# Performance work log

Measured on AMD Instinct MI355X. Metric: run time of the kernel, lower is better.

## Reference

```python
import jax, jax.numpy as jnp
import numpy as np

H = 8
LN_EPS = 1e-5

def setup_inputs() -> dict:
    key = jax.random.key(0)
    k1, k2, k3, k4 = jax.random.split(key, 4)
    bh, q_len, dk = 64, 1024, 64
    return {
        "query": jax.random.normal(k1, (bh, q_len, dk), dtype=jnp.float32),
        "key": jax.random.normal(k2, (bh, q_len, dk), dtype=jnp.float32),
        "value": jax.random.normal(k3, (bh, q_len, dk), dtype=jnp.float32),
        "head_att": jax.random.normal(k4, (H, H), dtype=jnp.float32),
        "ln_w": jnp.ones((H,), dtype=jnp.float32),
        "ln_b": jnp.zeros((H,), dtype=jnp.float32),
    }

def reference(query, key, value, head_att, ln_w, ln_b):
    bh, q_len, dk = query.shape
    k_len = key.shape[1]
    # scores: (bh, q, k)
    scores = jnp.einsum("bqd,bkd->bqk", query, key) / jnp.sqrt(jnp.asarray(dk, query.dtype))
    attn = jax.nn.softmax(scores, axis=-1)
    # view as (B, H, q, k) then move heads last: (B, q, k, H)
    a = attn.reshape(-1, H, q_len, k_len).transpose(0, 2, 3, 1)
    # DeepViT re-attention: cross-head mixing matmul
    a = a @ head_att  # (B, q, k, H)
    # LayerNorm over head dim
    mu = a.mean(axis=-1, keepdims=True)
    var = ((a - mu) ** 2).mean(axis=-1, keepdims=True)
    a = (a - mu) * jax.lax.rsqrt(var + LN_EPS) * ln_w + ln_b
    # back to (B, H, q, k)
    a = a.transpose(0, 3, 1, 2)
    att_map = a.mean(axis=1)  # (B, q, k)
    attention = a.reshape(bh, q_len, k_len)
    out = jnp.einsum("bqk,bkd->bqd", attention, value)
    return (out, att_map)
```

## Files before the change

### kernel.cpp

```cpp
#include <hip/hip_runtime.h>
#include <hip/hip_bf16.h>

typedef _Float16 f16;
typedef f16 f16x8 __attribute__((ext_vector_type(8)));
typedef f16 f16x4 __attribute__((ext_vector_type(4)));
typedef float f32x4 __attribute__((ext_vector_type(4)));

#define QL 1024
#define KL 1024
#define DKD 64
#define NH 8
#define LNEPS 1e-5f

__global__ __launch_bounds__(256) void prep_kf(const float* __restrict__ K, f16* __restrict__ kf) {
  int i = (blockIdx.x * 256 + threadIdx.x) * 4;
  float4 v = *reinterpret_cast<const float4*>(K + i);
  f16x4 o;
  o[0] = (f16)v.x; o[1] = (f16)v.y; o[2] = (f16)v.z; o[3] = (f16)v.w;
  *reinterpret_cast<f16x4*>(kf + i) = o;
}

__global__ __launch_bounds__(256) void prep_vt(const float* __restrict__ V, f16* __restrict__ vt) {
  __shared__ float t[32][33];
  const int bh = blockIdx.z, k0 = blockIdx.x * 32, d0 = blockIdx.y * 32;
  const float* src = V + ((size_t)bh * KL + k0) * DKD + d0;
#pragma unroll
  for (int j = 0; j < 4; ++j) {
    int kk = threadIdx.y * 4 + j;
    t[kk][threadIdx.x] = src[kk * DKD + threadIdx.x];
  }
  __syncthreads();
  f16* dst = vt + ((size_t)bh * DKD + d0) * KL + k0;
#pragma unroll
  for (int j = 0; j < 4; ++j) {
    int dd = threadIdx.y * 4 + j;
    dst[dd * KL + threadIdx.x] = (f16)t[threadIdx.x][dd];
  }
}

__global__ __launch_bounds__(256, 2) void main_kernel(
    const float* __restrict__ Qm, const f16* __restrict__ kf, const f16* __restrict__ vt,
    const float* __restrict__ hA, const float* __restrict__ lnw, const float* __restrict__ lnb,
    float* __restrict__ outp, float* __restrict__ att_map) {
  __shared__ __align__(16) f16 y_lds[2][NH][16][64];
  __shared__ float rs_lds[4][NH][16];

  const int tid = threadIdx.x;
  const int lane = tid & 63, w = tid >> 6;
  const int m = lane & 15, g = lane >> 4;
  const int b = blockIdx.y, q0 = blockIdx.x * 16;

  float haR[64], wR[8], bR[8];
#pragma unroll
  for (int j = 0; j < 64; ++j) haR[j] = hA[j];
#pragma unroll
  for (int j = 0; j < 8; ++j) { wR[j] = lnw[j]; bR[j] = lnb[j]; }

  f16x8 qf[NH][2];
#pragma unroll
  for (int h = 0; h < NH; ++h)
#pragma unroll
    for (int dc = 0; dc < 2; ++dc) {
      const float* qp = Qm + (((size_t)(b * NH + h)) * QL + q0 + m) * DKD + dc * 32 + g * 8;
      float4 a = *reinterpret_cast<const float4*>(qp);
      float4 c = *reinterpret_cast<const float4*>(qp + 4);
      f16x8 q;
      q[0] = (f16)(a.x * 0.125f); q[1] = (f16)(a.y * 0.125f);
      q[2] = (f16)(a.z * 0.125f); q[3] = (f16)(a.w * 0.125f);
      q[4] = (f16)(c.x * 0.125f); q[5] = (f16)(c.y * 0.125f);
      q[6] = (f16)(c.z * 0.125f); q[7] = (f16)(c.w * 0.125f);
      qf[h][dc] = q;
    }

  const size_t kbase_b = (size_t)b * NH * KL;

  float prs[NH][4];
#pragma unroll
  for (int h = 0; h < NH; ++h)
#pragma unroll
    for (int ri = 0; ri < 4; ++ri) prs[h][ri] = 0.f;

  for (int t = 0; t < 16; ++t) {
    const int k0 = w * 256 + t * 16;
    const f16* kb = kf + (kbase_b + k0 + m) * DKD + g * 8;
#pragma unroll
    for (int h = 0; h < NH; ++h) {
      f16x8 k0f = *reinterpret_cast<const f16x8*>(kb + (size_t)h * KL * DKD);
      f16x8 k1f = *reinterpret_cast<const f16x8*>(kb + (size_t)h * KL * DKD + 32);
      f32x4 acc = {0.f, 0.f, 0.f, 0.f};
      acc = __builtin_amdgcn_mfma_f32_16x16x32_f16(qf[h][0], k0f, acc, 0, 0, 0);
      acc = __builtin_amdgcn_mfma_f32_16x16x32_f16(qf[h][1], k1f, acc, 0, 0, 0);
#pragma unroll
      for (int ri = 0; ri < 4; ++ri) prs[h][ri] += __expf(acc[ri]);
    }
  }
#pragma unroll
  for (int h = 0; h < NH; ++h)
#pragma unroll
    for (int ri = 0; ri < 4; ++ri) {
      float v = prs[h][ri];
      v += __shfl_xor(v, 1); v += __shfl_xor(v, 2);
      v += __shfl_xor(v, 4); v += __shfl_xor(v, 8);
      prs[h][ri] = v;
    }
  if (m == 0) {
#pragma unroll
    for (int h = 0; h < NH; ++h)
#pragma unroll
      for (int ri = 0; ri < 4; ++ri) rs_lds[w][h][g * 4 + ri] = prs[h][ri];
  }
  __syncthreads();
  float inv_rs[NH][4];
#pragma unroll
  for (int h = 0; h < NH; ++h)
#pragma unroll
    for (int ri = 0; ri < 4; ++ri) {
      int qq = g * 4 + ri;
      inv_rs[h][ri] = 1.0f / (rs_lds[0][h][qq] + rs_lds[1][h][qq] +
                              rs_lds[2][h][qq] + rs_lds[3][h][qq]);
    }

  f32x4 oacc[2][4];
#pragma unroll
  for (int hp = 0; hp < 2; ++hp)
#pragma unroll
    for (int dt = 0; dt < 4; ++dt) oacc[hp][dt] = (f32x4){0.f, 0.f, 0.f, 0.f};

  for (int kt = 0; kt < 16; ++kt) {
    const int kbase = kt * 64;
    const int kcol = kbase + w * 16;
    const int buf = kt & 1;

    f32x4 pacc[NH];
    {
      const f16* kb = kf + (kbase_b + kcol + m) * DKD + g * 8;
#pragma unroll
      for (int h = 0; h < NH; ++h) {
        f16x8 k0f = *reinterpret_cast<const f16x8*>(kb + (size_t)h * KL * DKD);
        f16x8 k1f = *reinterpret_cast<const f16x8*>(kb + (size_t)h * KL * DKD + 32);
        f32x4 acc = {0.f, 0.f, 0.f, 0.f};
        acc = __builtin_amdgcn_mfma_f32_16x16x32_f16(qf[h][0], k0f, acc, 0, 0, 0);
        acc = __builtin_amdgcn_mfma_f32_16x16x32_f16(qf[h][1], k1f, acc, 0, 0, 0);
        pacc[h] = acc;
      }
    }
#pragma unroll
    for (int h = 0; h < NH; ++h)
#pragma unroll
      for (int ri = 0; ri < 4; ++ri)
        pacc[h][ri] = __expf(pacc[h][ri]) * inv_rs[h][ri];

#pragma unroll
    for (int ri = 0; ri < 4; ++ri) {
      const int qq = g * 4 + ri;
      float mixed[8];
      float mu = 0.f;
#pragma unroll
      for (int hh = 0; hh < 8; ++hh) {
        float s = 0.f;
#pragma unroll
        for (int j = 0; j < 8; ++j) s = fmaf(pacc[j][ri], haR[j * 8 + hh], s);
        mixed[hh] = s; mu += s;
      }
      mu *= 0.125f;
      float var = 0.f;
#pragma unroll
      for (int hh = 0; hh < 8; ++hh) { float d = mixed[hh] - mu; var = fmaf(d, d, var); }
      var *= 0.125f;
      const float rsv = rsqrtf(var + LNEPS);
      float am = 0.f;
      const int kidx = ((((2 * w + (m >> 3)) ^ (qq & 7)) << 3) | (m & 7));
#pragma unroll
      for (int hh = 0; hh < 8; ++hh) {
        float y = (mixed[hh] - mu) * rsv * wR[hh] + bR[hh];
        am += y;
        y_lds[buf][hh][qq][kidx] = (f16)y;
      }
      att_map[((size_t)b * QL + q0 + qq) * KL + kcol + m] = am * 0.125f;
    }
    __syncthreads();

#pragma unroll
    for (int hp = 0; hp < 2; ++hp) {
      const int hh = w + hp * 4;
      const f16* vb = vt + (((size_t)(b * NH + hh)) * DKD + m) * KL + kbase + g * 8;
#pragma unroll
      for (int ks = 0; ks < 2; ++ks) {
        const f16x8 af = *reinterpret_cast<const f16x8*>(
            &y_lds[buf][hh][m][((ks * 4 + g) ^ (m & 7)) << 3]);
#pragma unroll
        for (int dt = 0; dt < 4; ++dt) {
          f16x8 vf = *reinterpret_cast<const f16x8*>(vb + (size_t)dt * 16 * KL + ks * 32);
          oacc[hp][dt] = __builtin_amdgcn_mfma_f32_16x16x32_f16(af, vf, oacc[hp][dt], 0, 0, 0);
        }
      }
    }
  }

#pragma unroll
  for (int hp = 0; hp < 2; ++hp) {
    const int hh = w + hp * 4;
#pragma unroll
    for (int dt = 0; dt < 4; ++dt)
#pragma unroll
      for (int ri = 0; ri < 4; ++ri)
        outp[(((size_t)(b * NH + hh)) * QL + q0 + g * 4 + ri) * DKD + dt * 16 + m] =
            oacc[hp][dt][ri];
  }
}

extern "C" void kernel_launch(void* const* d_in, const int* in_sizes, int n_in,
                              void* d_out, int out_size, void* d_ws, size_t ws_size,
                              hipStream_t stream) {
  const float* Qm  = (const float*)d_in[0];
  const float* Km  = (const float*)d_in[1];
  const float* Vm  = (const float*)d_in[2];
  const float* hA  = (const float*)d_in[3];
  const float* lnw = (const float*)d_in[4];
  const float* lnb = (const float*)d_in[5];
  float* outp = (float*)d_out;
  float* att_map = outp + (size_t)64 * QL * DKD;

  char* ws = (char*)d_ws;
  f16* kfp = (f16*)ws;
  f16* vtp = (f16*)(ws + (size_t)8 * 1024 * 1024);

  prep_kf<<<4096, 256, 0, stream>>>(Km, kfp);
  prep_vt<<<dim3(32, 2, 64), dim3(32, 8), 0, stream>>>(Vm, vtp);
  main_kernel<<<dim3(64, 8), 256, 0, stream>>>(Qm, kfp, vtp, hA, lnw, lnb, outp, att_map);
}
```

Baseline: 211.7 us.

## Split softmax row-sum into separate kernel and split main kernel over key halves

Moves the softmax denominator pass into a standalone stats kernel with 1024 blocks, one per (bh, 64-row) tile, instead of having each main block recompute it. The main kernel now splits the key range in two across blocks, so there are 1024 blocks with a higher occupancy hint. The second half writes partial outputs to workspace and a reduce kernel adds them. This targets the low block count (512) of the old main kernel, at the cost of two extra launches and extra global traffic for the partial outputs and row sums.

```diff
diff --git a/kernel.cpp b/kernel.cpp
--- a/kernel.cpp
+++ b/kernel.cpp
@@ -38,17 +38,65 @@
   }
 }
 
-__global__ __launch_bounds__(256, 2) void main_kernel(
-    const float* __restrict__ Qm, const f16* __restrict__ kf, const f16* __restrict__ vt,
-    const float* __restrict__ hA, const float* __restrict__ lnw, const float* __restrict__ lnb,
-    float* __restrict__ outp, float* __restrict__ att_map) {
-  __shared__ __align__(16) f16 y_lds[2][NH][16][64];
-  __shared__ float rs_lds[4][NH][16];
-
+__global__ __launch_bounds__(256) void stats_kernel(const float* __restrict__ Qm,
+    const f16* __restrict__ kf, float* __restrict__ rowsum) {
   const int tid = threadIdx.x;
   const int lane = tid & 63, w = tid >> 6;
   const int m = lane & 15, g = lane >> 4;
-  const int b = blockIdx.y, q0 = blockIdx.x * 16;
+  const int id = blockIdx.x;
+  const int bh = (id & 7) * 8 + ((id >> 3) & 7);
+  const int q0 = (id >> 6) * 64 + w * 16;
+
+  f16x8 qf[2];
+#pragma unroll
+  for (int dc = 0; dc < 2; ++dc) {
+    const float* qp = Qm + ((size_t)bh * QL + q0 + m) * DKD + dc * 32 + g * 8;
+    float4 a = *reinterpret_cast<const float4*>(qp);
+    float4 c = *reinterpret_cast<const float4*>(qp + 4);
+    f16x8 q;
+    q[0] = (f16)(a.x * 0.125f); q[1] = (f16)(a.y * 0.125f);
+    q[2] = (f16)(a.z * 0.125f); q[3] = (f16)(a.w * 0.125f);
+    q[4] = (f16)(c.x * 0.125f); q[5] = (f16)(c.y * 0.125f);
+    q[6] = (f16)(c.z * 0.125f); q[7] = (f16)(c.w * 0.125f);
+    qf[dc] = q;
+  }
+  float part[4] = {0.f, 0.f, 0.f, 0.f};
+#pragma unroll 2
+  for (int kt = 0; kt < 64; ++kt) {
+    const f16* kb = kf + ((size_t)bh * KL + kt * 16 + m) * DKD + g * 8;
+    f16x8 k0f = *reinterpret_cast<const f16x8*>(kb);
+    f16x8 k1f = *reinterpret_cast<const f16x8*>(kb + 32);
+    f32x4 acc = {0.f, 0.f, 0.f, 0.f};
+    acc = __builtin_amdgcn_mfma_f32_16x16x32_f16(qf[0], k0f, acc, 0, 0, 0);
+    acc = __builtin_amdgcn_mfma_f32_16x16x32_f16(qf[1], k1f, acc, 0, 0, 0);
+#pragma unroll
+    for (int ri = 0; ri < 4; ++ri) part[ri] += __expf(acc[ri]);
+  }
+#pragma unroll
+  for (int ri = 0; ri < 4; ++ri) {
+    float v = part[ri];
+    v += __shfl_xor(v, 1); v += __shfl_xor(v, 2);
+    v += __shfl_xor(v, 4); v += __shfl_xor(v, 8);
+    part[ri] = v;
+  }
+  if (m == 0) {
+#pragma unroll
+    for (int ri = 0; ri < 4; ++ri) rowsum[(size_t)bh * QL + q0 + g * 4 + ri] = part[ri];
+  }
+}
+
+__global__ __launch_bounds__(256, 4) void main_kernel(
+    const float* __restrict__ Qm, const f16* __restrict__ kf, const f16* __restrict__ vt,
+    const float* __restrict__ rowsum,
+    const float* __restrict__ hA, const float* __restrict__ lnw, const float* __restrict__ lnb,
+    float* __restrict__ outp, float* __restrict__ part1, float* __restrict__ att_map) {
+  __shared__ __align__(16) f16 y_lds[2][NH][16][64];
+
+  const int tid = threadIdx.x;
+  const int lane = tid & 63, w = tid >> 6;
+  const int m = lane & 15, g = lane >> 4;
+  const int id = blockIdx.x;
+  const int b = id & 7, kc = (id >> 3) & 1, q0 = (id >> 4) * 16;
 
   float haR[64], wR[8], bR[8];
 #pragma unroll
@@ -71,63 +119,22 @@
       q[6] = (f16)(c.z * 0.125f); q[7] = (f16)(c.w * 0.125f);
       qf[h][dc] = q;
     }
+  float inv_rs[NH][4];
+#pragma unroll
+  for (int h = 0; h < NH; ++h)
+#pragma unroll
+    for (int ri = 0; ri < 4; ++ri)
+      inv_rs[h][ri] = 1.0f / rowsum[(size_t)(b * NH + h) * QL + q0 + g * 4 + ri];
 
   const size_t kbase_b = (size_t)b * NH * KL;
-
-  float prs[NH][4];
-#pragma unroll
-  for (int h = 0; h < NH; ++h)
-#pragma unroll
-    for (int ri = 0; ri < 4; ++ri) prs[h][ri] = 0.f;
-
-  for (int t = 0; t < 16; ++t) {
-    const int k0 = w * 256 + t * 16;
-    const f16* kb = kf + (kbase_b + k0 + m) * DKD + g * 8;
-#pragma unroll
-    for (int h = 0; h < NH; ++h) {
-      f16x8 k0f = *reinterpret_cast<const f16x8*>(kb + (size_t)h * KL * DKD);
-      f16x8 k1f = *reinterpret_cast<const f16x8*>(kb + (size_t)h * KL * DKD + 32);
-      f32x4 acc = {0.f, 0.f, 0.f, 0.f};
-      acc = __builtin_amdgcn_mfma_f32_16x16x32_f16(qf[h][0], k0f, acc, 0, 0, 0);
-      acc = __builtin_amdgcn_mfma_f32_16x16x32_f16(qf[h][1], k1f, acc, 0, 0, 0);
-#pragma unroll
-      for (int ri = 0; ri < 4; ++ri) prs[h][ri] += __expf(acc[ri]);
-    }
-  }
-#pragma unroll
-  for (int h = 0; h < NH; ++h)
-#pragma unroll
-    for (int ri = 0; ri < 4; ++ri) {
-      float v = prs[h][ri];
-      v += __shfl_xor(v, 1); v += __shfl_xor(v, 2);
-      v += __shfl_xor(v, 4); v += __shfl_xor(v, 8);
-      prs[h][ri] = v;
-    }
-  if (m == 0) {
-#pragma unroll
-    for (int h = 0; h < NH; ++h)
-#pragma unroll
-      for (int ri = 0; ri < 4; ++ri) rs_lds[w][h][g * 4 + ri] = prs[h][ri];
-  }
-  __syncthreads();
-  float inv_rs[NH][4];
-#pragma unroll
-  for (int h = 0; h < NH; ++h)
-#pragma unroll
-    for (int ri = 0; ri < 4; ++ri) {
-      int qq = g * 4 + ri;
-      inv_rs[h][ri] = 1.0f / (rs_lds[0][h][qq] + rs_lds[1][h][qq] +
-                              rs_lds[2][h][qq] + rs_lds[3][h][qq]);
-    }
-
   f32x4 oacc[2][4];
 #pragma unroll
   for (int hp = 0; hp < 2; ++hp)
 #pragma unroll
     for (int dt = 0; dt < 4; ++dt) oacc[hp][dt] = (f32x4){0.f, 0.f, 0.f, 0.f};
 
-  for (int kt = 0; kt < 16; ++kt) {
-    const int kbase = kt * 64;
+  for (int kt = 0; kt < 8; ++kt) {
+    const int kbase = kc * 512 + kt * 64;
     const int kcol = kbase + w * 16;
     const int buf = kt & 1;
 
@@ -197,6 +204,7 @@
     }
   }
 
+  float* dst = kc ? part1 : outp;
 #pragma unroll
   for (int hp = 0; hp < 2; ++hp) {
     const int hh = w + hp * 4;
@@ -204,9 +212,18 @@
     for (int dt = 0; dt < 4; ++dt)
 #pragma unroll
       for (int ri = 0; ri < 4; ++ri)
-        outp[(((size_t)(b * NH + hh)) * QL + q0 + g * 4 + ri) * DKD + dt * 16 + m] =
+        dst[(((size_t)(b * NH + hh)) * QL + q0 + g * 4 + ri) * DKD + dt * 16 + m] =
             oacc[hp][dt][ri];
   }
+}
+
+__global__ __launch_bounds__(256) void reduce_kernel(const float* __restrict__ p1,
+                                                     float* __restrict__ outp) {
+  size_t i = ((size_t)blockIdx.x * 256 + threadIdx.x) * 4;
+  float4 a = *reinterpret_cast<const float4*>(outp + i);
+  float4 c = *reinterpret_cast<const float4*>(p1 + i);
+  a.x += c.x; a.y += c.y; a.z += c.z; a.w += c.w;
+  *reinterpret_cast<float4*>(outp + i) = a;
 }
 
 extern "C" void kernel_launch(void* const* d_in, const int* in_sizes, int n_in,
@@ -222,10 +239,14 @@
   float* att_map = outp + (size_t)64 * QL * DKD;
 
   char* ws = (char*)d_ws;
-  f16* kfp = (f16*)ws;
-  f16* vtp = (f16*)(ws + (size_t)8 * 1024 * 1024);
+  f16* kfp   = (f16*)ws;
+  f16* vtp   = (f16*)(ws + (size_t)8388608);
+  float* rsm = (float*)(ws + (size_t)16777216);
+  float* p1  = (float*)(ws + (size_t)17039360);
 
   prep_kf<<<4096, 256, 0, stream>>>(Km, kfp);
   prep_vt<<<dim3(32, 2, 64), dim3(32, 8), 0, stream>>>(Vm, vtp);
-  main_kernel<<<dim3(64, 8), 256, 0, stream>>>(Qm, kfp, vtp, hA, lnw, lnb, outp, att_map);
-}
+  stats_kernel<<<1024, 256, 0, stream>>>(Qm, kfp, rsm);
+  main_kernel<<<1024, 256, 0, stream>>>(Qm, kfp, vtp, rsm, hA, lnw, lnb, outp, p1, att_map);
+  reduce_kernel<<<4096, 256, 0, stream>>>(p1, outp);
+}
```

Result: slower. 289.8 us (+36.9%).
